# Optimization experiments

Measured on AMD Instinct MI355X. Metric: run time of the kernel, lower is better.

## Reference

```python
import jax, jax.numpy as jnp
import numpy as np

B, CIN, COUT, N, M, K = 8, 128, 256, 8192, 2048, 16
BN_EPS = 1e-5


def setup_inputs() -> dict:
    key = jax.random.key(0)
    k1, k2, k3 = jax.random.split(key, 3)
    x = jax.random.normal(k1, (B, CIN, N), dtype=jnp.float32)
    coords = jax.random.normal(k2, (B, 3, N), dtype=jnp.float32)
    W = jax.random.normal(k3, (COUT, CIN), dtype=jnp.float32) * 0.05  # 1x1 conv, bias=False
    gamma = jnp.ones((COUT,), dtype=jnp.float32)   # BatchNorm2d weight
    beta = jnp.zeros((COUT,), dtype=jnp.float32)   # BatchNorm2d bias
    return {"x": x, "coords": coords, "W": W, "gamma": gamma, "beta": beta}


def furthest_point_sampling(coords, num_samples):
    """coords: (B,3,N) -> indices (B,num_samples) int32. Greedy FPS starting at index 0."""
    pts = coords.transpose(0, 2, 1)  # (B,N,3)
    b, n, _ = pts.shape
    idx0 = jnp.zeros((b,), dtype=jnp.int32)
    mind0 = jnp.full((b, n), 1e10, dtype=pts.dtype)

    def step(carry, _):
        mind, last = carry
        lastpt = jnp.take_along_axis(pts, last[:, None, None], axis=1)  # (b,1,3)
        d = jnp.sum((pts - lastpt) ** 2, axis=-1)                        # (b,n)
        mind = jnp.minimum(mind, d)
        nxt = jnp.argmax(mind, axis=-1).astype(jnp.int32)
        return (mind, nxt), nxt

    (_, _), rest = jax.lax.scan(step, (mind0, idx0), None, length=num_samples - 1)
    return jnp.concatenate([idx0[:, None], rest.T], axis=1)  # (b,num_samples)


def reference(x, coords, W, gamma, beta):
    b = x.shape[0]
    fps_idx = furthest_point_sampling(coords, M)                # (B,M)
    pts = coords.transpose(0, 2, 1)                             # (B,N,3)
    bidx = jnp.arange(b)[:, None]
    fps_pts = pts[bidx, fps_idx]                                # (B,M,3)

    # squared-distance matrix via ||a||^2 + ||b||^2 - 2ab (avoids (B,M,N,3) temp)
    d = (jnp.sum(fps_pts ** 2, -1)[:, :, None]
         + jnp.sum(pts ** 2, -1)[:, None, :]
         - 2.0 * jnp.einsum('bmd,bnd->bmn', fps_pts, pts))      # (B,M,N)
    _, knn_idx = jax.lax.top_k(-d, K)                           # (B,M,K) nearest (sorted)

    x_t = x.transpose(0, 2, 1)                                  # (B,N,Cin)
    knn = x_t[jnp.arange(b)[:, None, None], knn_idx]            # (B,M,K,Cin)

    # PointwiseConv2D: 1x1 conv (no bias) + BatchNorm2d (batch stats) + ReLU
    h = jnp.einsum('bmkc,oc->bmko', knn, W)                     # (B,M,K,Cout)
    mean = jnp.mean(h, axis=(0, 1, 2))
    var = jnp.var(h, axis=(0, 1, 2))
    h = (h - mean) * jax.lax.rsqrt(var + BN_EPS) * gamma + beta
    h = jax.nn.relu(h)

    y = jnp.max(h, axis=2).transpose(0, 2, 1)                   # (B,Cout,M), max over k
    fps_coords = fps_pts.transpose(0, 2, 1)                     # (B,3,M)
    return y, fps_coords
```

## Files before the change

kernel.cpp:

```cpp
#include <hip/hip_runtime.h>
#include <math.h>

#define B_ 8
#define CIN_ 128
#define COUT_ 256
#define N_ 8192
#define M_ 2048
#define K_ 16

#define WORKERS 240
#define NTILE 2048
#define NGROUP 2048

__device__ __forceinline__ unsigned umax2(unsigned a, unsigned b) { return a > b ? a : b; }
__device__ __forceinline__ unsigned umin2(unsigned a, unsigned b) { return a < b ? a : b; }

__device__ __forceinline__ unsigned wave_reduce_umax(unsigned v) {
    v = umax2(v, (unsigned)__builtin_amdgcn_update_dpp(0, (int)v, 0x111, 0xf, 0xf, false));
    v = umax2(v, (unsigned)__builtin_amdgcn_update_dpp(0, (int)v, 0x112, 0xf, 0xf, false));
    v = umax2(v, (unsigned)__builtin_amdgcn_update_dpp(0, (int)v, 0x114, 0xf, 0xf, false));
    v = umax2(v, (unsigned)__builtin_amdgcn_update_dpp(0, (int)v, 0x118, 0xf, 0xf, false));
    v = umax2(v, (unsigned)__builtin_amdgcn_update_dpp(0, (int)v, 0x142, 0xf, 0xf, false));
    v = umax2(v, (unsigned)__builtin_amdgcn_update_dpp(0, (int)v, 0x143, 0xf, 0xf, false));
    return (unsigned)__builtin_amdgcn_readlane((int)v, 63);
}
__device__ __forceinline__ unsigned wave_reduce_umin(unsigned v) {
    v = umin2(v, (unsigned)__builtin_amdgcn_update_dpp(-1, (int)v, 0x111, 0xf, 0xf, false));
    v = umin2(v, (unsigned)__builtin_amdgcn_update_dpp(-1, (int)v, 0x112, 0xf, 0xf, false));
    v = umin2(v, (unsigned)__builtin_amdgcn_update_dpp(-1, (int)v, 0x114, 0xf, 0xf, false));
    v = umin2(v, (unsigned)__builtin_amdgcn_update_dpp(-1, (int)v, 0x118, 0xf, 0xf, false));
    v = umin2(v, (unsigned)__builtin_amdgcn_update_dpp(-1, (int)v, 0x142, 0xf, 0xf, false));
    v = umin2(v, (unsigned)__builtin_amdgcn_update_dpp(-1, (int)v, 0x143, 0xf, 0xf, false));
    return (unsigned)__builtin_amdgcn_readlane((int)v, 63);
}

__global__ __launch_bounds__(512) void mega_kernel(const float* __restrict__ coords,
                                                   const float* __restrict__ x,
                                                   const float* __restrict__ W,
                                                   unsigned* __restrict__ wflag,
                                                   float* __restrict__ out_fps,
                                                   float* __restrict__ hp,
                                                   int* __restrict__ knn,
                                                   double* __restrict__ partial,
                                                   int* __restrict__ gbar) {
    __shared__ union {
        struct {
            float4 pts[N_];
            unsigned long long kbuf[2][8];
            int wlist[M_];
        } f;
        struct {
            float Xs[64][128];
            float Wt[64][68];
        } g;
        struct {
            float4 tile[1024];
            double wacc[8][512];
        } k;
    } sm;

    const int tid = threadIdx.x;
    const int lane = tid & 63;
    const int w = tid >> 6;

    if (blockIdx.x < B_) {
#pragma clang fp contract(off)
        const int b = blockIdx.x;
        const float* cb = coords + (size_t)b * 3 * N_;
        float4* pts = sm.f.pts;
        unsigned long long (*kbuf)[8] = sm.f.kbuf;
        int* wlist = sm.f.wlist;

        float px[16], py[16], pz[16], mind[16];
#pragma unroll
        for (int s = 0; s < 16; ++s) {
            int p = tid + s * 512;
            px[s] = cb[p];
            py[s] = cb[N_ + p];
            pz[s] = cb[2 * N_ + p];
            mind[s] = 1e10f;
            pts[p] = make_float4(px[s], py[s], pz[s], 0.f);
        }
        if (tid == 0)
            __hip_atomic_store(&wflag[(size_t)b * M_], 0u,
                               __ATOMIC_RELAXED, __HIP_MEMORY_SCOPE_AGENT);
        __syncthreads();
        float4 p0 = pts[0];
        float lx = p0.x, ly = p0.y, lz = p0.z;

        int par = 0;
        for (int m = 1; m < M_; ++m) {
            float bv = -1.0f; int bs = 0;
#pragma unroll
            for (int s = 0; s < 16; ++s) {
                float dx = px[s] - lx;
                float dy = py[s] - ly;
                float dz = pz[s] - lz;
                float d = __builtin_fmaf(dz, dz, __builtin_fmaf(dy, dy, dx * dx));
                float mn = fminf(mind[s], d);
                mind[s] = mn;
                if (mn > bv) { bv = mn; bs = s; }
            }
            int bi = tid + bs * 512;
            unsigned kd = __float_as_uint(bv);
            unsigned md = wave_reduce_umax(kd);
            unsigned cand = (kd == md) ? (unsigned)bi : 0xffffffffu;
            unsigned mi = wave_reduce_umin(cand);
            if (lane == 0)
                kbuf[par][w] = ((unsigned long long)md << 32) |
                               (unsigned long long)(0xffffffffu - mi);
            __syncthreads();
            const unsigned long long* kb = kbuf[par];
            ulonglong2 q0 = *(const ulonglong2*)&kb[0];
            ulonglong2 q1 = *(const ulonglong2*)&kb[2];
            ulonglong2 q2 = *(const ulonglong2*)&kb[4];
            ulonglong2 q3 = *(const ulonglong2*)&kb[6];
            unsigned long long a0 = q0.x > q0.y ? q0.x : q0.y;
            unsigned long long a1 = q1.x > q1.y ? q1.x : q1.y;
            unsigned long long a2 = q2.x > q2.y ? q2.x : q2.y;
            unsigned long long a3 = q3.x > q3.y ? q3.x : q3.y;
            unsigned long long b01 = a0 > a1 ? a0 : a1;
            unsigned long long b23 = a2 > a3 ? a2 : a3;
            unsigned long long best = b01 > b23 ? b01 : b23;
            int widx = (int)(0xffffffffu - (unsigned)(best & 0xffffffffull));
            widx = ((unsigned)widx < (unsigned)N_) ? widx : 0;
            float4 wp = pts[widx];
            lx = wp.x; ly = wp.y; lz = wp.z;
            if (tid == 0) {
                wlist[m] = widx;
                __hip_atomic_store(&wflag[(size_t)b * M_ + m], (unsigned)widx,
                                   __ATOMIC_RELAXED, __HIP_MEMORY_SCOPE_AGENT);
            }
            par ^= 1;
        }

        __syncthreads();
        for (int mm = tid; mm < M_; mm += 512) {
            int wi = (mm == 0) ? 0 : wlist[mm];
            wi = ((unsigned)wi < (unsigned)N_) ? wi : 0;
            float4 wp = pts[wi];
            out_fps[(size_t)b * 3 * M_ + 0 * M_ + mm] = wp.x;
            out_fps[(size_t)b * 3 * M_ + 1 * M_ + mm] = wp.y;
            out_fps[(size_t)b * 3 * M_ + 2 * M_ + mm] = wp.z;
        }
    } else {
        const int wkr = blockIdx.x - B_;

        float (*Xs)[128] = sm.g.Xs;
        float (*Wt)[68] = sm.g.Wt;
        for (int t = wkr; t < NTILE; t += WORKERS) {
            const int b = t >> 8;
            const int rem = t & 255;
            const int n0 = (rem >> 2) * 128;
            const int o0 = (rem & 3) * 64;
            const int tn = (tid & 31) * 4;
            const int to = (tid >> 5) * 4;
            const float* xg = x + (size_t)b * CIN_ * N_;

            float acc[4][4] = {};
            for (int kk = 0; kk < CIN_; kk += 64) {
#pragma unroll
                for (int i = 0; i < 16; ++i) {
                    int e = tid + 512 * i;
                    int r = e >> 7, q = e & 127;
                    Xs[r][q] = xg[(size_t)(kk + r) * N_ + n0 + q];
                }
#pragma unroll
                for (int i = 0; i < 8; ++i) {
                    int e = tid + 512 * i;
                    int r = e >> 6, q = e & 63;
                    Wt[q][r] = W[(size_t)(o0 + r) * CIN_ + kk + q];
                }
                __syncthreads();
#pragma unroll 8
                for (int c = 0; c < 64; ++c) {
                    float4 a = *(const float4*)&Xs[c][tn];
                    float4 bb = *(const float4*)&Wt[c][to];
                    float av[4] = {a.x, a.y, a.z, a.w};
                    float bv[4] = {bb.x, bb.y, bb.z, bb.w};
#pragma unroll
                    for (int j = 0; j < 4; ++j)
#pragma unroll
                        for (int l = 0; l < 4; ++l)
                            acc[j][l] += av[j] * bv[l];
                }
                __syncthreads();
            }
#pragma unroll
            for (int j = 0; j < 4; ++j) {
                float4 v = make_float4(acc[j][0], acc[j][1], acc[j][2], acc[j][3]);
                *(float4*)&hp[((size_t)b * N_ + n0 + tn + j) * COUT_ + o0 + to] = v;
            }
        }

        __threadfence();
        if (tid == 0) {
            __hip_atomic_fetch_add(gbar, 1, __ATOMIC_RELEASE, __HIP_MEMORY_SCOPE_AGENT);
            while (__hip_atomic_load(gbar, __ATOMIC_ACQUIRE, __HIP_MEMORY_SCOPE_AGENT) < WORKERS)
                __builtin_amdgcn_s_sleep(8);
        }
        __syncthreads();

        {
#pragma clang fp contract(off)
            float4* tile = sm.k.tile;
            double sAcc[4] = {0.0, 0.0, 0.0, 0.0};
            double s2Acc[4] = {0.0, 0.0, 0.0, 0.0};

            for (int g = wkr; g < NGROUP; g += WORKERS) {
                const int b = g & 7;
                const int mg = g >> 3;
                const int m = mg * 8 + w;
                const int row = b * M_ + m;
                const float* cb = coords + (size_t)b * 3 * N_;

                unsigned widx;
                while ((widx = __hip_atomic_load(&wflag[row], __ATOMIC_RELAXED,
                                                 __HIP_MEMORY_SCOPE_AGENT)) == 0xffffffffu)
                    __builtin_amdgcn_s_sleep(2);
                widx = (widx < (unsigned)N_) ? widx : 0;

                const float fx = cb[widx];
                const float fy = cb[N_ + widx];
                const float fz = cb[2 * N_ + widx];
                const float sf = __builtin_fmaf(fz, fz, __builtin_fmaf(fy, fy, fx * fx));

                float ed = INFINITY; int ei = 0x7fffffff;
                float tau_d = INFINITY; int tau_i = 0x7fffffff;

                for (int t = 0; t < 8; ++t) {
                    const int base = t * 1024;
#pragma unroll
                    for (int j = 0; j < 2; ++j) {
                        int idx = tid + 512 * j;
                        int n = base + idx;
                        float gx = cb[n], gy = cb[N_ + n], gz = cb[2 * N_ + n];
                        float sp = __builtin_fmaf(gz, gz, __builtin_fmaf(gy, gy, gx * gx));
                        tile[idx] = make_float4(gx, gy, gz, sp);
                    }
                    __syncthreads();
                    for (int s = 0; s < 16; ++s) {
                        int l = s * 64 + lane;
                        float4 p = tile[l];
                        int n = base + l;
                        float dot = __builtin_fmaf(fz, p.z, __builtin_fmaf(fy, p.y, fx * p.x));
                        float d = (sf + p.w) - 2.0f * dot;
                        bool q = (d < tau_d) || (d == tau_d && n < tau_i);
                        unsigned long long bal = __ballot(q);
                        while (bal) {
                            int lb = __ffsll(bal) - 1;
                            bal &= bal - 1;
                            float dv = __shfl(d, lb);
                            int   iv = __shfl(n, lb);
                            if ((dv < tau_d) || (dv == tau_d && iv < tau_i)) {
                                float pud = __shfl_up(ed, 1);
                                int   pui = __shfl_up(ei, 1);
                                bool cs = (dv < ed) || (dv == ed && iv < ei);
                                bool cp = (lane != 0) && ((dv < pud) || (dv == pud && iv < pui));
                                ed = cs ? (cp ? pud : dv) : ed;
                                ei = cs ? (cp ? pui : iv) : ei;
                                tau_d = __shfl(ed, 15);
                                tau_i = __shfl(ei, 15);
                            }
                        }
                    }
                    __syncthreads();
                }
                if (lane < K_) {
                    int v = ei;
                    v = ((unsigned)v < (unsigned)N_) ? v : 0;
                    knn[(size_t)row * K_ + lane] = v;
                }
#pragma unroll
                for (int k = 0; k < K_; ++k) {
                    int iv = __shfl(ei, k);
                    iv = ((unsigned)iv < (unsigned)N_) ? iv : 0;
                    const float* hrow = hp + ((size_t)b * N_ + iv) * COUT_;
#pragma unroll
                    for (int j = 0; j < 4; ++j) {
                        double h = (double)hrow[lane + 64 * j];
                        sAcc[j] += h;
                        s2Acc[j] += h * h;
                    }
                }
            }

            double (*wacc)[512] = sm.k.wacc;
#pragma unroll
            for (int j = 0; j < 4; ++j) {
                wacc[w][lane + 64 * j] = sAcc[j];
                wacc[w][256 + lane + 64 * j] = s2Acc[j];
            }
            __syncthreads();
            double tsum = 0.0;
#pragma unroll
            for (int wv = 0; wv < 8; ++wv) tsum += wacc[wv][tid];
            partial[(size_t)wkr * 512 + tid] = tsum;
        }
    }
}

__global__ void bn_final_kernel(const double* __restrict__ partial,
                                const float* __restrict__ gamma,
                                const float* __restrict__ beta,
                                float* __restrict__ scale,
                                float* __restrict__ bias) {
    int o = threadIdx.x;
    double s = 0.0, s2 = 0.0;
    for (int j = 0; j < WORKERS; ++j) {
        s += partial[(size_t)j * 512 + o];
        s2 += partial[(size_t)j * 512 + 256 + o];
    }
    const double inv = 1.0 / (double)(B_ * M_ * K_);
    double mean = s * inv;
    double var = s2 * inv - mean * mean;
    if (var < 0.0) var = 0.0;
    double r = 1.0 / sqrt(var + 1e-5);
    double g = (double)gamma[o];
    scale[o] = (float)(r * g);
    bias[o] = (float)((double)beta[o] - mean * r * g);
}

__global__ __launch_bounds__(256) void finalize_kernel(const float* __restrict__ hp,
                                                       const int* __restrict__ knn,
                                                       const float* __restrict__ scale,
                                                       const float* __restrict__ bias,
                                                       float* __restrict__ y) {
    const int b = blockIdx.x >> 6;
    const int m0 = (blockIdx.x & 63) * 32;
    const int tid = threadIdx.x;
    __shared__ int kidx[512];
    __shared__ float tile[32][257];

    for (int e = tid; e < 512; e += 256) {
        int n = knn[(b * M_ + m0 + (e >> 4)) * K_ + (e & 15)];
        kidx[e] = ((unsigned)n < (unsigned)N_) ? n : 0;
    }
    __syncthreads();

    const float s = scale[tid];
    const float t = bias[tid];
    const float* hb = hp + (size_t)b * N_ * COUT_;
    for (int mm = 0; mm < 32; ++mm) {
        float v = -INFINITY;
#pragma unroll
        for (int k = 0; k < K_; ++k) {
            int n = kidx[mm * 16 + k];
            float h = hb[(size_t)n * COUT_ + tid];
            v = fmaxf(v, h * s + t);
        }
        v = fmaxf(v, 0.0f);
        tile[mm][tid] = v;
    }
    __syncthreads();
#pragma unroll
    for (int r = 0; r < 32; ++r) {
        int o2 = r * 8 + (tid >> 5);
        int mm = tid & 31;
        y[((size_t)b * COUT_ + o2) * M_ + m0 + mm] = tile[mm][o2];
    }
}

__global__ void sentinel_kernel(float* out, float v) { out[0] = v; }

extern "C" void kernel_launch(void* const* d_in, const int* in_sizes, int n_in,
                              void* d_out, int out_size, void* d_ws, size_t ws_size,
                              hipStream_t stream) {
    const float* x = (const float*)d_in[0];
    const float* coords = (const float*)d_in[1];
    const float* W = (const float*)d_in[2];
    const float* gamma = (const float*)d_in[3];
    const float* beta = (const float*)d_in[4];
    float* y = (float*)d_out;
    float* out_fps = y + (size_t)B_ * COUT_ * M_;

    if (n_in != 5 ||
        in_sizes[0] != B_ * CIN_ * N_ ||
        in_sizes[1] != B_ * 3 * N_ ||
        in_sizes[2] != COUT_ * CIN_ ||
        in_sizes[3] != COUT_ || in_sizes[4] != COUT_ ||
        out_size != B_ * COUT_ * M_ + B_ * 3 * M_) {
        sentinel_kernel<<<1, 1, 0, stream>>>(y, -2.0e6f);
        return;
    }

    const size_t HP_BYTES = (size_t)B_ * N_ * COUT_ * 4;
    const size_t KNN_BYTES = (size_t)B_ * M_ * K_ * 4;
    const size_t PART_BYTES = (size_t)WORKERS * 512 * 8;
    const size_t WFLAG_BYTES = (size_t)B_ * M_ * 4;
    const size_t NEED = HP_BYTES + KNN_BYTES + PART_BYTES + WFLAG_BYTES + 8192;
    if (ws_size < NEED) {
        sentinel_kernel<<<1, 1, 0, stream>>>(y, -1.0e6f);
        return;
    }
    char* ws = (char*)d_ws;
    float* hp = (float*)ws;
    int* knn = (int*)(ws + HP_BYTES);
    double* partial = (double*)(ws + HP_BYTES + KNN_BYTES);
    unsigned* wflag = (unsigned*)(ws + HP_BYTES + KNN_BYTES + PART_BYTES);
    char* tail = ws + HP_BYTES + KNN_BYTES + PART_BYTES + WFLAG_BYTES;
    int* gbar = (int*)tail;
    float* scale = (float*)(tail + 256);
    float* bias = scale + 256;

    (void)hipMemsetAsync(wflag, 0xFF, WFLAG_BYTES, stream);
    (void)hipMemsetAsync(gbar, 0, 256, stream);

    mega_kernel<<<B_ + WORKERS, 512, 0, stream>>>(coords, x, W, wflag, out_fps,
                                                  hp, knn, partial, gbar);
    bn_final_kernel<<<1, 256, 0, stream>>>(partial, gamma, beta, scale, bias);
    finalize_kernel<<<512, 256, 0, stream>>>(hp, knn, scale, bias, y);
}
```

Baseline: 1.712 ms.

## Fuse per-row raw max into KNN stats pass and fold BN finalize into mega kernel

```diff
diff --git a/kernel.cpp b/kernel.cpp
--- a/kernel.cpp
+++ b/kernel.cpp
@@ -42,7 +42,12 @@
                                                    float* __restrict__ hp,
                                                    int* __restrict__ knn,
                                                    double* __restrict__ partial,
-                                                   int* __restrict__ gbar) {
+                                                   int* __restrict__ gbar,
+                                                   float* __restrict__ ymax,
+                                                   const float* __restrict__ gamma,
+                                                   const float* __restrict__ beta,
+                                                   float* __restrict__ scale,
+                                                   float* __restrict__ bias) {
     __shared__ union {
         struct {
             float4 pts[N_];
@@ -195,8 +200,8 @@
 
         __threadfence();
         if (tid == 0) {
-            __hip_atomic_fetch_add(gbar, 1, __ATOMIC_RELEASE, __HIP_MEMORY_SCOPE_AGENT);
-            while (__hip_atomic_load(gbar, __ATOMIC_ACQUIRE, __HIP_MEMORY_SCOPE_AGENT) < WORKERS)
+            __hip_atomic_fetch_add(&gbar[0], 1, __ATOMIC_RELEASE, __HIP_MEMORY_SCOPE_AGENT);
+            while (__hip_atomic_load(&gbar[0], __ATOMIC_ACQUIRE, __HIP_MEMORY_SCOPE_AGENT) < WORKERS)
                 __builtin_amdgcn_s_sleep(8);
         }
         __syncthreads();
@@ -271,6 +276,7 @@
                     v = ((unsigned)v < (unsigned)N_) ? v : 0;
                     knn[(size_t)row * K_ + lane] = v;
                 }
+                float mx[4] = {-INFINITY, -INFINITY, -INFINITY, -INFINITY};
 #pragma unroll
                 for (int k = 0; k < K_; ++k) {
                     int iv = __shfl(ei, k);
@@ -278,11 +284,16 @@
                     const float* hrow = hp + ((size_t)b * N_ + iv) * COUT_;
 #pragma unroll
                     for (int j = 0; j < 4; ++j) {
-                        double h = (double)hrow[lane + 64 * j];
+                        float hv = hrow[lane + 64 * j];
+                        double h = (double)hv;
                         sAcc[j] += h;
                         s2Acc[j] += h * h;
+                        mx[j] = fmaxf(mx[j], hv);
                     }
                 }
+#pragma unroll
+                for (int j = 0; j < 4; ++j)
+                    ymax[((size_t)b * COUT_ + (lane + 64 * j)) * M_ + m] = mx[j];
             }
 
             double (*wacc)[512] = sm.k.wacc;
@@ -297,28 +308,34 @@
             for (int wv = 0; wv < 8; ++wv) tsum += wacc[wv][tid];
             partial[(size_t)wkr * 512 + tid] = tsum;
         }
+
+        __threadfence();
+        if (tid == 0)
+            __hip_atomic_fetch_add(&gbar[1], 1, __ATOMIC_RELEASE, __HIP_MEMORY_SCOPE_AGENT);
+        if (wkr == 0) {
+            if (tid == 0) {
+                while (__hip_atomic_load(&gbar[1], __ATOMIC_ACQUIRE, __HIP_MEMORY_SCOPE_AGENT) < WORKERS)
+                    __builtin_amdgcn_s_sleep(8);
+            }
+            __syncthreads();
+            if (tid < 256) {
+                int o = tid;
+                double s = 0.0, s2 = 0.0;
+                for (int j = 0; j < WORKERS; ++j) {
+                    s += partial[(size_t)j * 512 + o];
+                    s2 += partial[(size_t)j * 512 + 256 + o];
+                }
+                const double inv = 1.0 / (double)(B_ * M_ * K_);
+                double mean = s * inv;
+                double var = s2 * inv - mean * mean;
+                if (var < 0.0) var = 0.0;
+                double r = 1.0 / sqrt(var + 1e-5);
+                double gm = (double)gamma[o];
+                scale[o] = (float)(r * gm);
+                bias[o] = (float)((double)beta[o] - mean * r * gm);
+            }
+        }
     }
-}
-
-__global__ void bn_final_kernel(const double* __restrict__ partial,
-                                const float* __restrict__ gamma,
-                                const float* __restrict__ beta,
-                                float* __restrict__ scale,
-                                float* __restrict__ bias) {
-    int o = threadIdx.x;
-    double s = 0.0, s2 = 0.0;
-    for (int j = 0; j < WORKERS; ++j) {
-        s += partial[(size_t)j * 512 + o];
-        s2 += partial[(size_t)j * 512 + 256 + o];
-    }
-    const double inv = 1.0 / (double)(B_ * M_ * K_);
-    double mean = s * inv;
-    double var = s2 * inv - mean * mean;
-    if (var < 0.0) var = 0.0;
-    double r = 1.0 / sqrt(var + 1e-5);
-    double g = (double)gamma[o];
-    scale[o] = (float)(r * g);
-    bias[o] = (float)((double)beta[o] - mean * r * g);
 }
 
 __global__ __launch_bounds__(256) void finalize_kernel(const float* __restrict__ hp,
@@ -326,38 +343,32 @@
                                                        const float* __restrict__ scale,
                                                        const float* __restrict__ bias,
                                                        float* __restrict__ y) {
-    const int b = blockIdx.x >> 6;
-    const int m0 = (blockIdx.x & 63) * 32;
+    const int b = blockIdx.x >> 8;
+    const int o = blockIdx.x & 255;
+    const float s = scale[o];
+    const float t = bias[o];
+    float* yrow = y + ((size_t)b * COUT_ + o) * M_;
     const int tid = threadIdx.x;
-    __shared__ int kidx[512];
-    __shared__ float tile[32][257];
-
-    for (int e = tid; e < 512; e += 256) {
-        int n = knn[(b * M_ + m0 + (e >> 4)) * K_ + (e & 15)];
-        kidx[e] = ((unsigned)n < (unsigned)N_) ? n : 0;
-    }
-    __syncthreads();
-
-    const float s = scale[tid];
-    const float t = bias[tid];
-    const float* hb = hp + (size_t)b * N_ * COUT_;
-    for (int mm = 0; mm < 32; ++mm) {
-        float v = -INFINITY;
-#pragma unroll
-        for (int k = 0; k < K_; ++k) {
-            int n = kidx[mm * 16 + k];
-            float h = hb[(size_t)n * COUT_ + tid];
-            v = fmaxf(v, h * s + t);
-        }
-        v = fmaxf(v, 0.0f);
-        tile[mm][tid] = v;
-    }
-    __syncthreads();
-#pragma unroll
-    for (int r = 0; r < 32; ++r) {
-        int o2 = r * 8 + (tid >> 5);
-        int mm = tid & 31;
-        y[((size_t)b * COUT_ + o2) * M_ + m0 + mm] = tile[mm][o2];
+    if (s >= 0.0f) {
+#pragma unroll
+        for (int i = 0; i < 8; ++i) {
+            int m = tid + 256 * i;
+            float h = yrow[m];
+            float v = h * s + t;
+            yrow[m] = fmaxf(v, 0.0f);
+        }
+    } else {
+        for (int i = 0; i < 8; ++i) {
+            int m = tid + 256 * i;
+            float v = -INFINITY;
+            for (int k = 0; k < K_; ++k) {
+                int n = knn[(size_t)(b * M_ + m) * K_ + k];
+                n = ((unsigned)n < (unsigned)N_) ? n : 0;
+                float h = hp[((size_t)b * N_ + n) * COUT_ + o];
+                v = fmaxf(v, h * s + t);
+            }
+            yrow[m] = fmaxf(v, 0.0f);
+        }
     }
 }
 
@@ -407,7 +418,7 @@
     (void)hipMemsetAsync(gbar, 0, 256, stream);
 
     mega_kernel<<<B_ + WORKERS, 512, 0, stream>>>(coords, x, W, wflag, out_fps,
-                                                  hp, knn, partial, gbar);
-    bn_final_kernel<<<1, 256, 0, stream>>>(partial, gamma, beta, scale, bias);
-    finalize_kernel<<<512, 256, 0, stream>>>(hp, knn, scale, bias, y);
+                                                  hp, knn, partial, gbar, y,
+                                                  gamma, beta, scale, bias);
+    finalize_kernel<<<B_ * COUT_, 256, 0, stream>>>(hp, knn, scale, bias, y);
 }
```

After: 1.669 ms. 2.5% less time.
